# Performance work log

Hardware: AMD Instinct MI355X
Metric: run time of the kernel (lower is better)

## Reference

```python
import jax, jax.numpy as jnp
import numpy as np

NUM_BUCKETS = 32
MAX_DISTANCE = 128
N_HEADS = 16
D_KV = 64


def relative_position_bucket(rel, num_buckets=NUM_BUCKETS, max_distance=MAX_DISTANCE):
    # bidirectional (encoder) bucketing, matches the torch reference
    nb = num_buckets // 2
    ret = (rel > 0).astype(jnp.int32) * nb
    rp = jnp.abs(rel)
    max_exact = nb // 2
    is_small = rp < max_exact
    # guard log(0); masked out by is_small anyway
    large = max_exact + (
        jnp.log(jnp.maximum(rp, 1).astype(jnp.float32) / max_exact)
        / np.log(max_distance / max_exact)
        * (nb - max_exact)
    ).astype(jnp.int32)
    large = jnp.minimum(large, nb - 1)
    return ret + jnp.where(is_small, rp, large)


def compute_bias(rel_bias_table, q_len, k_len):
    q_pos = jnp.arange(q_len)[:, None]
    k_pos = jnp.arange(k_len)[None, :]
    buckets = relative_position_bucket(k_pos - q_pos)  # [S, K]
    bias = rel_bias_table[buckets]                      # [S, K, H]
    return jnp.transpose(bias, (2, 0, 1))[None]         # [1, H, S, K]


def setup_inputs() -> dict:
    key = jax.random.key(0)
    ks = jax.random.split(key, 6)
    d_model, inner = 1024, N_HEADS * D_KV
    scale = 1.0 / np.sqrt(d_model)
    return {
        "hidden_states": jax.random.normal(ks[0], (4, 2048, d_model), jnp.float32),
        "Wq": jax.random.normal(ks[1], (d_model, inner), jnp.float32) * scale,
        "Wk": jax.random.normal(ks[2], (d_model, inner), jnp.float32) * scale,
        "Wv": jax.random.normal(ks[3], (d_model, inner), jnp.float32) * scale,
        "Wo": jax.random.normal(ks[4], (inner, d_model), jnp.float32) * scale,
        "rel_bias_table": jax.random.normal(ks[5], (NUM_BUCKETS, N_HEADS), jnp.float32),
    }


def reference(hidden_states, Wq, Wk, Wv, Wo, rel_bias_table):
    B, S, _ = hidden_states.shape
    K_len = S  # self-attention (key_value_states is None)
    q = (hidden_states @ Wq).reshape(B, S, N_HEADS, D_KV)
    k = (hidden_states @ Wk).reshape(B, K_len, N_HEADS, D_KV)
    v = (hidden_states @ Wv).reshape(B, K_len, N_HEADS, D_KV)
    # NOTE: T5 attention has no 1/sqrt(d_kv) scaling
    scores = jnp.einsum("bshd,bkhd->bhsk", q, k)
    pos_bias = compute_bias(rel_bias_table, S, K_len)
    attn = jax.nn.softmax(scores + pos_bias, axis=-1)
    out = jnp.einsum("bhsk,bkhd->bshd", attn, v).reshape(B, S, N_HEADS * D_KV)
    out = out @ Wo
    return (out, pos_bias)
```

## Files before the change

### kernel.cpp

```cpp
#include <hip/hip_runtime.h>
#include <cstdint>
#include <cstddef>

typedef unsigned short u16;
typedef unsigned int u32;
typedef __attribute__((ext_vector_type(8))) short bf16x8;
typedef __attribute__((ext_vector_type(4))) float f32x4;

#define MFMA(a, b, c) __builtin_amdgcn_mfma_f32_16x16x32_bf16((a), (b), (c), 0, 0, 0)

typedef const __attribute__((address_space(1))) void gv1_t;
typedef __attribute__((address_space(3))) void lv3_t;
#define GLOAD_LDS16(g, l) __builtin_amdgcn_global_load_lds((gv1_t*)(g), (lv3_t*)(l), 16, 0, 0)

#define BATCH 4
#define SEQ 2048
#define DMODEL 1024
#define NHEAD 16
#define MROWS (BATCH * SEQ)
#define QKVN (3 * DMODEL)

#define LOG2E 1.44269504088896340736f

__device__ __forceinline__ u16 f2bf(float f) {
  u32 x = __builtin_bit_cast(u32, f);
  x += 0x7fffu + ((x >> 16) & 1u);
  return (u16)(x >> 16);
}

__device__ __forceinline__ u32 pkbf(float a, float b) {
  return (u32)f2bf(a) | ((u32)f2bf(b) << 16);
}

extern "C" __device__ float __ocml_exp2_f32(float);
__device__ __forceinline__ float exp2fast(float x) {
#if __has_builtin(__builtin_amdgcn_exp2f)
  return __builtin_amdgcn_exp2f(x);
#else
  return __ocml_exp2_f32(x);
#endif
}

__device__ __forceinline__ float xqmax(float v) {
  v = fmaxf(v, __shfl_xor(v, 16));
  return fmaxf(v, __shfl_xor(v, 32));
}
__device__ __forceinline__ float xqsum(float v) {
  v += __shfl_xor(v, 16);
  return v + __shfl_xor(v, 32);
}

__global__ __launch_bounds__(256) void convert_h(const float* __restrict__ H,
                                                 u16* __restrict__ Hb) {
  size_t i = (size_t)blockIdx.x * 1024 + threadIdx.x * 4;
  float4 v = *(const float4*)&H[i];
  uint2 o;
  o.x = pkbf(v.x, v.y);
  o.y = pkbf(v.z, v.w);
  *(uint2*)&Hb[i] = o;
}

__global__ void transpose_w(const float* __restrict__ Wq, const float* __restrict__ Wk,
                            const float* __restrict__ Wv, const float* __restrict__ Wo,
                            u16* __restrict__ Wt) {
  __shared__ u16 Ts[32][33];
  const float* W = (blockIdx.z == 0) ? Wq : (blockIdx.z == 1) ? Wk
                   : (blockIdx.z == 2) ? Wv : Wo;
  const float s = (blockIdx.z == 0) ? LOG2E : 1.0f;
  int x = threadIdx.x, y0 = threadIdx.y;
  int r0 = blockIdx.y * 32, c0 = blockIdx.x * 32;
  for (int yy = y0; yy < 32; yy += 8)
    Ts[yy][x] = f2bf(W[(size_t)(r0 + yy) * 1024 + c0 + x] * s);
  __syncthreads();
  for (int yy = y0; yy < 32; yy += 8)
    Wt[(size_t)(blockIdx.z * 1024 + c0 + yy) * 1024 + r0 + x] = Ts[x][yy];
}

__device__ __forceinline__ int rel_bucket(int rel) {
  int ret = (rel > 0) ? 16 : 0;
  int rp = (rel < 0) ? -rel : rel;
  if (rp < 8) return ret + rp;
  int i = 0;
  i += (rp >= 12); i += (rp >= 16); i += (rp >= 23); i += (rp >= 32);
  i += (rp >= 46); i += (rp >= 64); i += (rp >= 91);
  return ret + 8 + i;
}

__global__ __launch_bounds__(256) void build_bias_rel(const float* __restrict__ tbl,
                                                      float* __restrict__ brel,
                                                      float* __restrict__ brel2) {
  int h = blockIdx.x;
  for (int rix = threadIdx.x; rix < 4095; rix += 256) {
    float v = tbl[rel_bucket(rix - 2047) * NHEAD + h];
    brel[h * 4096 + rix] = v;
    brel2[h * 4096 + rix] = v * LOG2E;
  }
}

__global__ __launch_bounds__(256) void write_pos_bias(const float* __restrict__ brel,
                                                      float* __restrict__ pb) {
  int s = blockIdx.x, h = blockIdx.y;
  const float* br = brel + h * 4096 + 2047 - s;
  float* o = pb + ((size_t)h * SEQ + s) * SEQ;
  #pragma unroll
  for (int p = 0; p < 2; ++p) {
    int k = (threadIdx.x + p * 256) * 4;
    float4 v;
    v.x = br[k]; v.y = br[k + 1]; v.z = br[k + 2]; v.w = br[k + 3];
    *(float4*)&o[k] = v;
  }
}

__global__ __launch_bounds__(256) void gemm_bf16k(const u16* __restrict__ A,
                                                  const u16* __restrict__ Bt,
                                                  u16* __restrict__ Cb, float* __restrict__ Cf,
                                                  int M, int N, int K) {
  __shared__ u16 As[128 * 32];
  __shared__ u16 Bs[128 * 32];
  const int t = threadIdx.x;
  const int w = t >> 6, lane = t & 63, quad = lane >> 4, l15 = lane & 15;
  const int wr = w >> 1, wc = w & 1;
  const int row0 = blockIdx.y * 128, col0 = blockIdx.x * 128;

  f32x4 acc[4][4];
  #pragma unroll
  for (int i = 0; i < 4; ++i)
    #pragma unroll
    for (int j = 0; j < 4; ++j) acc[i][j] = (f32x4){0.f, 0.f, 0.f, 0.f};

  const int srow = lane >> 2, scol = (lane & 3) * 8;

  for (int k0 = 0; k0 < K; k0 += 32) {
    #pragma unroll
    for (int p = 0; p < 2; ++p) {
      const int rb = w * 32 + p * 16;
      GLOAD_LDS16(&A[(size_t)(row0 + rb + srow) * K + k0 + scol], &As[rb * 32]);
      GLOAD_LDS16(&Bt[(size_t)(col0 + rb + srow) * K + k0 + scol], &Bs[rb * 32]);
    }
    __syncthreads();
    bf16x8 af[4], bfr[4];
    #pragma unroll
    for (int i = 0; i < 4; ++i)
      af[i] = *(const bf16x8*)&As[(wr * 64 + i * 16 + l15) * 32 + quad * 8];
    #pragma unroll
    for (int j = 0; j < 4; ++j)
      bfr[j] = *(const bf16x8*)&Bs[(wc * 64 + j * 16 + l15) * 32 + quad * 8];
    #pragma unroll
    for (int i = 0; i < 4; ++i)
      #pragma unroll
      for (int j = 0; j < 4; ++j)
        acc[i][j] = MFMA(af[i], bfr[j], acc[i][j]);
    __syncthreads();
  }
  #pragma unroll
  for (int i = 0; i < 4; ++i) {
    #pragma unroll
    for (int j = 0; j < 4; ++j) {
      int col = col0 + wc * 64 + j * 16 + l15;
      #pragma unroll
      for (int r = 0; r < 4; ++r) {
        int row = row0 + wr * 64 + i * 16 + quad * 4 + r;
        if (Cb) Cb[(size_t)row * N + col] = f2bf(acc[i][j][r]);
        else    Cf[(size_t)row * N + col] = acc[i][j][r];
      }
    }
  }
}

__global__ __launch_bounds__(256) void transpose_v(const u16* __restrict__ QKV,
                                                   u16* __restrict__ Vt) {
  __shared__ u16 Ts[64 * 72];
  int st = blockIdx.x, bh = blockIdx.y;
  int b = bh >> 4, h = bh & 15;
  int t = threadIdx.x;
  #pragma unroll
  for (int p = 0; p < 2; ++p) {
    int c = t * 2 + p, r = c >> 3, cc = (c & 7) * 8;
    *(uint4*)&Ts[r * 72 + cc] =
        *(const uint4*)&QKV[(size_t)(b * SEQ + st * 64 + r) * QKVN + 2 * DMODEL + h * 64 + cc];
  }
  __syncthreads();
  #pragma unroll
  for (int p = 0; p < 2; ++p) {
    int c = t * 2 + p, d = c >> 3, s8 = (c & 7) * 8;
    union { u16 u[8]; uint4 v; } tmp;
    #pragma unroll
    for (int jj = 0; jj < 8; ++jj) tmp.u[jj] = Ts[(s8 + jj) * 72 + d];
    *(uint4*)&Vt[((size_t)(bh * 64 + d)) * SEQ + st * 64 + s8] = tmp.v;
  }
}

__global__ __launch_bounds__(256) void attn_fused(const u16* __restrict__ QKV,
                                                  const u16* __restrict__ Vt,
                                                  const float* __restrict__ brel2,
                                                  u16* __restrict__ Aout) {
  __shared__ u16 Ks[64 * 72];
  __shared__ u16 Vs[64 * 72];
  __shared__ u16 Ps[4][16 * 72];
  const int qt = blockIdx.x, bh = blockIdx.y;
  const int b = bh >> 4, h = bh & 15;
  const int t = threadIdx.x;
  const int w = t >> 6, lane = t & 63, quad = lane >> 4, l15 = lane & 15;
  const int q0 = qt * 64 + w * 16;

  const float cpos = brel2[h * 4096 + 4040];
  const float cneg = brel2[h * 4096 + 54];

  const u16* qptr = QKV + (size_t)(b * SEQ + q0 + l15) * QKVN + h * 64 + quad * 8;
  bf16x8 aq0 = *(const bf16x8*)qptr;
  bf16x8 aq1 = *(const bf16x8*)(qptr + 32);

  float mrow = -1e30f, lrow = 0.f;
  f32x4 oacc[4];
  #pragma unroll
  for (int j = 0; j < 4; ++j) oacc[j] = (f32x4){0.f, 0.f, 0.f, 0.f};

  const int c0 = t * 2, c1 = c0 + 1;
  const int r0s = c0 >> 3, cc0 = (c0 & 7) * 8;
  const int r1s = c1 >> 3, cc1 = (c1 & 7) * 8;
  const size_t krow = (size_t)(b * SEQ) * QKVN + DMODEL + h * 64;
  const size_t vtrow = (size_t)bh * 64;
  const float* brow = brel2 + h * 4096 + 2047;
  const int dbias = quad * 4 - q0 - l15;
  u16* Pw = Ps[w];

  for (int kb = 0; kb < SEQ; kb += 64) {
    *(uint4*)&Ks[r0s * 72 + cc0] = *(const uint4*)&QKV[krow + (size_t)(kb + r0s) * QKVN + cc0];
    *(uint4*)&Ks[r1s * 72 + cc1] = *(const uint4*)&QKV[krow + (size_t)(kb + r1s) * QKVN + cc1];
    *(uint4*)&Vs[r0s * 72 + cc0] = *(const uint4*)&Vt[(vtrow + r0s) * SEQ + kb + cc0];
    *(uint4*)&Vs[r1s * 72 + cc1] = *(const uint4*)&Vt[(vtrow + r1s) * SEQ + kb + cc1];
    __syncthreads();

    f32x4 sc[4];
    #pragma unroll
    for (int j = 0; j < 4; ++j) {
      bf16x8 bk0 = *(const bf16x8*)&Ks[(j * 16 + l15) * 72 + quad * 8];
      bf16x8 bk1 = *(const bf16x8*)&Ks[(j * 16 + l15) * 72 + 32 + quad * 8];
      f32x4 z = (f32x4){0.f, 0.f, 0.f, 0.f};
      z = MFMA(bk0, aq0, z);
      z = MFMA(bk1, aq1, z);
      sc[j] = z;
    }

    const bool fastp = (kb >= q0 + 106);
    const bool fastn = (kb + 154 <= q0);
    const float cb = fastp ? cpos : (fastn ? cneg : 0.f);
    if (!(fastp || fastn)) {
      #pragma unroll
      for (int j = 0; j < 4; ++j)
        #pragma unroll
        for (int r = 0; r < 4; ++r)
          sc[j][r] += brow[kb + j * 16 + r + dbias];
    }

    float tm = sc[0][0];
    #pragma unroll
    for (int j = 0; j < 4; ++j)
      #pragma unroll
      for (int r = 0; r < 4; ++r) tm = fmaxf(tm, sc[j][r]);
    tm = xqmax(tm);

    float mn = fmaxf(mrow, tm + cb);
    float alpha = exp2fast(mrow - mn);
    mrow = mn;
    const float mm = mn - cb;

    float ls = 0.f;
    #pragma unroll
    for (int j = 0; j < 4; ++j) {
      float p0 = exp2fast(sc[j][0] - mm);
      float p1 = exp2fast(sc[j][1] - mm);
      float p2 = exp2fast(sc[j][2] - mm);
      float p3 = exp2fast(sc[j][3] - mm);
      ls += (p0 + p1) + (p2 + p3);
      uint2 pk;
      pk.x = pkbf(p0, p1);
      pk.y = pkbf(p2, p3);
      *(uint2*)&Pw[l15 * 72 + j * 16 + quad * 4] = pk;
    }
    ls = xqsum(ls);
    lrow = lrow * alpha + ls;
    #pragma unroll
    for (int j = 0; j < 4; ++j) {
      oacc[j][0] *= alpha; oacc[j][1] *= alpha;
      oacc[j][2] *= alpha; oacc[j][3] *= alpha;
    }

    asm volatile("s_waitcnt lgkmcnt(0)" ::: "memory");
    bf16x8 bp0 = *(const bf16x8*)&Pw[l15 * 72 + quad * 8];
    bf16x8 bp1 = *(const bf16x8*)&Pw[l15 * 72 + 32 + quad * 8];
    #pragma unroll
    for (int j2 = 0; j2 < 4; ++j2) {
      bf16x8 av0 = *(const bf16x8*)&Vs[(j2 * 16 + l15) * 72 + quad * 8];
      bf16x8 av1 = *(const bf16x8*)&Vs[(j2 * 16 + l15) * 72 + 32 + quad * 8];
      oacc[j2] = MFMA(av0, bp0, oacc[j2]);
      oacc[j2] = MFMA(av1, bp1, oacc[j2]);
    }
    __syncthreads();
  }

  const float inv = 1.0f / lrow;
  const size_t rowb = (size_t)(b * SEQ + q0 + l15) * DMODEL + h * 64;
  #pragma unroll
  for (int j2 = 0; j2 < 4; ++j2) {
    uint2 o;
    o.x = pkbf(oacc[j2][0] * inv, oacc[j2][1] * inv);
    o.y = pkbf(oacc[j2][2] * inv, oacc[j2][3] * inv);
    *(uint2*)&Aout[rowb + j2 * 16 + quad * 4] = o;
  }
}

extern "C" void kernel_launch(void* const* d_in, const int* in_sizes, int n_in,
                              void* d_out, int out_size, void* d_ws, size_t ws_size,
                              hipStream_t stream) {
  (void)in_sizes; (void)n_in; (void)out_size; (void)ws_size;
  const float* H   = (const float*)d_in[0];
  const float* Wq  = (const float*)d_in[1];
  const float* Wk  = (const float*)d_in[2];
  const float* Wv  = (const float*)d_in[3];
  const float* Wo  = (const float*)d_in[4];
  const float* tbl = (const float*)d_in[5];

  float* out = (float*)d_out;
  float* pos_bias = out + (size_t)MROWS * DMODEL;

  char* ws = (char*)d_ws;
  u16* Hb     = (u16*)(ws);
  u16* Wt     = (u16*)(ws + 16777216);
  u16* QKV    = (u16*)(ws + 25165824);
  u16* Vt     = (u16*)(ws + 75497472);
  float* brel  = (float*)(ws + 92274688);
  float* brel2 = (float*)(ws + 92536832);

  convert_h<<<8192, 256, 0, stream>>>(H, Hb);
  transpose_w<<<dim3(32, 32, 4), dim3(32, 8), 0, stream>>>(Wq, Wk, Wv, Wo, Wt);
  build_bias_rel<<<16, 256, 0, stream>>>(tbl, brel, brel2);
  write_pos_bias<<<dim3(2048, 16), 256, 0, stream>>>(brel, pos_bias);

  gemm_bf16k<<<dim3(QKVN / 128, MROWS / 128), 256, 0, stream>>>(
      Hb, Wt, QKV, nullptr, MROWS, QKVN, DMODEL);
  transpose_v<<<dim3(32, 64), 256, 0, stream>>>(QKV, Vt);
  attn_fused<<<dim3(32, 64), 256, 0, stream>>>(QKV, Vt, brel2, Hb );
  gemm_bf16k<<<dim3(DMODEL / 128, MROWS / 128), 256, 0, stream>>>(
      Hb, Wt + (size_t)QKVN * DMODEL, nullptr, out, MROWS, DMODEL, DMODEL);
}
```

Before: 621.9 us.

## Fuse pos_bias output writes into attention kernel and register-prefetch K/V tiles

```diff
diff --git a/kernel.cpp b/kernel.cpp
--- a/kernel.cpp
+++ b/kernel.cpp
@@ -97,20 +97,6 @@
   }
 }
 
-__global__ __launch_bounds__(256) void write_pos_bias(const float* __restrict__ brel,
-                                                      float* __restrict__ pb) {
-  int s = blockIdx.x, h = blockIdx.y;
-  const float* br = brel + h * 4096 + 2047 - s;
-  float* o = pb + ((size_t)h * SEQ + s) * SEQ;
-  #pragma unroll
-  for (int p = 0; p < 2; ++p) {
-    int k = (threadIdx.x + p * 256) * 4;
-    float4 v;
-    v.x = br[k]; v.y = br[k + 1]; v.z = br[k + 2]; v.w = br[k + 3];
-    *(float4*)&o[k] = v;
-  }
-}
-
 __global__ __launch_bounds__(256) void gemm_bf16k(const u16* __restrict__ A,
                                                   const u16* __restrict__ Bt,
                                                   u16* __restrict__ Cb, float* __restrict__ Cf,
@@ -192,8 +178,10 @@
 
 __global__ __launch_bounds__(256) void attn_fused(const u16* __restrict__ QKV,
                                                   const u16* __restrict__ Vt,
+                                                  const float* __restrict__ brel,
                                                   const float* __restrict__ brel2,
-                                                  u16* __restrict__ Aout) {
+                                                  u16* __restrict__ Aout,
+                                                  float* __restrict__ pb) {
   __shared__ u16 Ks[64 * 72];
   __shared__ u16 Vs[64 * 72];
   __shared__ u16 Ps[4][16 * 72];
@@ -202,9 +190,12 @@
   const int t = threadIdx.x;
   const int w = t >> 6, lane = t & 63, quad = lane >> 4, l15 = lane & 15;
   const int q0 = qt * 64 + w * 16;
+  const bool wrbias = (bh < 16);
 
   const float cpos = brel2[h * 4096 + 4040];
   const float cneg = brel2[h * 4096 + 54];
+  const float cpu  = brel[h * 4096 + 4040];
+  const float cnu  = brel[h * 4096 + 54];
 
   const u16* qptr = QKV + (size_t)(b * SEQ + q0 + l15) * QKVN + h * 64 + quad * 8;
   bf16x8 aq0 = *(const bf16x8*)qptr;
@@ -224,12 +215,24 @@
   const int dbias = quad * 4 - q0 - l15;
   u16* Pw = Ps[w];
 
+  uint4 ka0 = *(const uint4*)&QKV[krow + (size_t)r0s * QKVN + cc0];
+  uint4 ka1 = *(const uint4*)&QKV[krow + (size_t)r1s * QKVN + cc1];
+  uint4 va0 = *(const uint4*)&Vt[(vtrow + r0s) * SEQ + cc0];
+  uint4 va1 = *(const uint4*)&Vt[(vtrow + r1s) * SEQ + cc1];
+
   for (int kb = 0; kb < SEQ; kb += 64) {
-    *(uint4*)&Ks[r0s * 72 + cc0] = *(const uint4*)&QKV[krow + (size_t)(kb + r0s) * QKVN + cc0];
-    *(uint4*)&Ks[r1s * 72 + cc1] = *(const uint4*)&QKV[krow + (size_t)(kb + r1s) * QKVN + cc1];
-    *(uint4*)&Vs[r0s * 72 + cc0] = *(const uint4*)&Vt[(vtrow + r0s) * SEQ + kb + cc0];
-    *(uint4*)&Vs[r1s * 72 + cc1] = *(const uint4*)&Vt[(vtrow + r1s) * SEQ + kb + cc1];
+    *(uint4*)&Ks[r0s * 72 + cc0] = ka0;
+    *(uint4*)&Ks[r1s * 72 + cc1] = ka1;
+    *(uint4*)&Vs[r0s * 72 + cc0] = va0;
+    *(uint4*)&Vs[r1s * 72 + cc1] = va1;
     __syncthreads();
+
+    if (kb + 64 < SEQ) {
+      ka0 = *(const uint4*)&QKV[krow + (size_t)(kb + 64 + r0s) * QKVN + cc0];
+      ka1 = *(const uint4*)&QKV[krow + (size_t)(kb + 64 + r1s) * QKVN + cc1];
+      va0 = *(const uint4*)&Vt[(vtrow + r0s) * SEQ + kb + 64 + cc0];
+      va1 = *(const uint4*)&Vt[(vtrow + r1s) * SEQ + kb + 64 + cc1];
+    }
 
     f32x4 sc[4];
     #pragma unroll
@@ -245,6 +248,26 @@
     const bool fastp = (kb >= q0 + 106);
     const bool fastn = (kb + 154 <= q0);
     const float cb = fastp ? cpos : (fastn ? cneg : 0.f);
+
+    if (wrbias) {
+      float* po = pb + ((size_t)(h * SEQ + q0 + l15)) * SEQ + kb + quad * 16;
+      if (fastp || fastn) {
+        const float c = fastp ? cpu : cnu;
+        const float4 vv = {c, c, c, c};
+        #pragma unroll
+        for (int i = 0; i < 4; ++i) *(float4*)&po[i * 4] = vv;
+      } else {
+        const float* bb = brel + h * 4096 + 2047 - (q0 + l15) + kb + quad * 16;
+        #pragma unroll
+        for (int i = 0; i < 4; ++i) {
+          float4 vv;
+          vv.x = bb[i * 4]; vv.y = bb[i * 4 + 1];
+          vv.z = bb[i * 4 + 2]; vv.w = bb[i * 4 + 3];
+          *(float4*)&po[i * 4] = vv;
+        }
+      }
+    }
+
     if (!(fastp || fastn)) {
       #pragma unroll
       for (int j = 0; j < 4; ++j)
@@ -335,12 +358,12 @@
   convert_h<<<8192, 256, 0, stream>>>(H, Hb);
   transpose_w<<<dim3(32, 32, 4), dim3(32, 8), 0, stream>>>(Wq, Wk, Wv, Wo, Wt);
   build_bias_rel<<<16, 256, 0, stream>>>(tbl, brel, brel2);
-  write_pos_bias<<<dim3(2048, 16), 256, 0, stream>>>(brel, pos_bias);
 
   gemm_bf16k<<<dim3(QKVN / 128, MROWS / 128), 256, 0, stream>>>(
       Hb, Wt, QKV, nullptr, MROWS, QKVN, DMODEL);
   transpose_v<<<dim3(32, 64), 256, 0, stream>>>(QKV, Vt);
-  attn_fused<<<dim3(32, 64), 256, 0, stream>>>(QKV, Vt, brel2, Hb );
+  attn_fused<<<dim3(32, 64), 256, 0, stream>>>(QKV, Vt, brel, brel2,
+                                               Hb , pos_bias);
   gemm_bf16k<<<dim3(DMODEL / 128, MROWS / 128), 256, 0, stream>>>(
       Hb, Wt + (size_t)QKVN * DMODEL, nullptr, out, MROWS, DMODEL, DMODEL);
 }
```

After: 617.3 us. Within noise of the previous version (-0.7%).
